# Optimization experiments

Hardware: AMD Instinct MI355X
Metric: run time of the kernel (lower is better)

The kernel has to match this reference:

```python
import jax, jax.numpy as jnp
import numpy as np

N, K, D = 65536, 16, 64  # points, neighbors, d_out
EPS = 1e-5


def setup_inputs() -> dict:
    key = jax.random.key(0)
    ks = jax.random.split(key, 10)
    s = lambda fan: 1.0 / np.sqrt(fan)
    return {
        "p": jax.random.normal(ks[0], (N, K, 3), jnp.float32),
        "x": jax.random.normal(ks[1], (N, K, D), jnp.float32),
        # BiMLP: Conv1d(10, 2D, 1) -> BN -> ReLU -> Conv1d(2D, D, 1)
        "w1": jax.random.normal(ks[2], (10, 2 * D), jnp.float32) * s(10),
        "b1": jnp.zeros((2 * D,), jnp.float32),
        "g1": jnp.ones((2 * D,), jnp.float32),
        "be1": jnp.zeros((2 * D,), jnp.float32),
        "w2": jax.random.normal(ks[3], (2 * D, D), jnp.float32) * s(2 * D),
        "b2": jnp.zeros((D,), jnp.float32),
        # score_fn: Linear(2D, 2D, bias=False)
        "ws": jax.random.normal(ks[4], (2 * D, 2 * D), jnp.float32) * s(2 * D),
        # mlp_out: Linear(2D, D) -> BN -> ReLU
        "wo": jax.random.normal(ks[5], (2 * D, D), jnp.float32) * s(2 * D),
        "bo": jnp.zeros((D,), jnp.float32),
        "g2": jnp.ones((D,), jnp.float32),
        "be2": jnp.zeros((D,), jnp.float32),
    }


def reference(p, x, w1, b1, g1, be1, w2, b2, ws, wo, bo, g2, be2):
    # p: [N,K,3] neighbor coords (index 0 is the center), x: [N,K,D]
    center = p[:, :1, :]                                   # [N,1,3]
    diff = center - p                                      # [N,K,3]
    dist = jnp.sqrt(jnp.sum(diff * diff, axis=2, keepdims=True))  # [N,K,1]
    concat = jnp.concatenate(
        [jnp.broadcast_to(center, p.shape), p, diff, dist], axis=-1)  # [N,K,10]

    # 1x1 conv == per-point linear over channel dim
    h = jnp.einsum('nkc,cd->nkd', concat, w1) + b1          # [N,K,2D]
    # BatchNorm1d over (N,K) per channel (training-mode batch stats)
    mu = jnp.mean(h, axis=(0, 1))
    var = jnp.var(h, axis=(0, 1))
    h = (h - mu) * jax.lax.rsqrt(var + EPS) * g1 + be1
    h = jax.nn.relu(h)
    p_c = jnp.einsum('nkd,de->nke', h, w2) + b2             # [N,K,D]

    p_x = jnp.concatenate([p_c, x], axis=-1)                # [N,K,2D]
    # attention scores: linear (no bias) then softmax over neighbor dim (-2)
    scores = jax.nn.softmax(jnp.einsum('nkd,de->nke', p_x, ws), axis=-2)
    feat = jnp.sum(scores * p_x, axis=1)                    # [N,2D]

    out = feat @ wo + bo                                    # [N,D]
    mu2 = jnp.mean(out, axis=0)
    var2 = jnp.var(out, axis=0)
    out = (out - mu2) * jax.lax.rsqrt(var2 + EPS) * g2 + be2
    return jax.nn.relu(out)
```

## Files before the change

### kernel.cpp

```cpp
#include <hip/hip_runtime.h>
#include <math.h>

#define NPTS 65536
#define EPSV 1e-5f
#define B1G  256
#define B3G  512

#define OFF_P1  0
#define OFF_S1  (B1G*65)
#define OFF_P2  (OFF_S1+256)
#define OFF_S2  (OFF_P2+B3G*128)
#define OFF_PRE (OFF_S2+128)

typedef unsigned int u32;
typedef short v8s __attribute__((ext_vector_type(8)));
typedef float v4f __attribute__((ext_vector_type(4)));

union F8 { v8s v; u32 u[4]; unsigned short s[8]; };

__device__ __forceinline__ u32 f2bf(float f){
  u32 u = __float_as_uint(f);
  return (u + 0x7fffu + ((u>>16)&1u)) >> 16;
}
__device__ __forceinline__ float bf2f(unsigned short s){ return __uint_as_float(((u32)s)<<16); }
__device__ __forceinline__ u32 packbf(float a, float b){ return f2bf(a) | (f2bf(b)<<16); }

__global__ __launch_bounds__(256) void k1_stats(const float* __restrict__ p, float* __restrict__ part1){
  int tid = blockIdx.x*256 + threadIdx.x;
  float M[55]; float s[10];
  #pragma unroll
  for(int i=0;i<55;i++) M[i]=0.f;
  #pragma unroll
  for(int i=0;i<10;i++) s[i]=0.f;
  for(int it=0; it<16; ++it){
    int r = it*65536 + tid;
    int n = r >> 4;
    int kk = r & 15;
    const float* pn = p + (size_t)n*48;
    float cx=pn[0], cy=pn[1], cz=pn[2];
    float ax=pn[kk*3+0], ay=pn[kk*3+1], az=pn[kk*3+2];
    float dx=cx-ax, dy=cy-ay, dz=cz-az;
    float dd = sqrtf(dx*dx+dy*dy+dz*dz);
    float c[10]={cx,cy,cz,ax,ay,az,dx,dy,dz,dd};
    #pragma unroll
    for(int i=0;i<10;i++) s[i]+=c[i];
    int idx=0;
    #pragma unroll
    for(int i=0;i<10;i++){
      #pragma unroll
      for(int j=i;j<10;j++){
        M[idx] = fmaf(c[i],c[j],M[idx]);
        idx++;
      }
    }
  }
  #pragma unroll
  for(int i=0;i<10;i++){
    for(int off=32; off>0; off>>=1) s[i] += __shfl_down(s[i], off, 64);
  }
  #pragma unroll
  for(int i=0;i<55;i++){
    for(int off=32; off>0; off>>=1) M[i] += __shfl_down(M[i], off, 64);
  }
  __shared__ float sm[4][65];
  int lane = threadIdx.x & 63, w = threadIdx.x >> 6;
  if(lane==0){
    #pragma unroll
    for(int i=0;i<10;i++) sm[w][i]=s[i];
    #pragma unroll
    for(int i=0;i<55;i++) sm[w][10+i]=M[i];
  }
  __syncthreads();
  if(threadIdx.x<65){
    float v = sm[0][threadIdx.x]+sm[1][threadIdx.x]+sm[2][threadIdx.x]+sm[3][threadIdx.x];
    part1[blockIdx.x*65 + threadIdx.x] = v;
  }
}

__device__ __forceinline__ int tri_idx(int i,int j){
  int a = i<j? i : j;
  int b = i<j? j : i;
  return 10*a - (a*(a-1))/2 + (b-a);
}
__global__ void k2_fin(const float* __restrict__ part1, const float* __restrict__ w1,
                       const float* __restrict__ g1, const float* __restrict__ be1,
                       float* __restrict__ stats1){
  __shared__ float S[65];
  int t = threadIdx.x;
  if(t<65){
    float a=0.f;
    for(int b=0;b<B1G;b++) a += part1[b*65+t];
    S[t]=a;
  }
  __syncthreads();
  float wc[10];
  #pragma unroll
  for(int c=0;c<10;c++) wc[c]=w1[c*128+t];
  float md=0.f;
  #pragma unroll
  for(int c=0;c<10;c++) md += S[c]*wc[c];
  const float invR = 1.0f/(float)(NPTS*16);
  md *= invR;
  float q=0.f;
  #pragma unroll
  for(int i=0;i<10;i++){
    float ti=0.f;
    #pragma unroll
    for(int j=0;j<10;j++) ti += S[10+tri_idx(i,j)]*wc[j];
    q = fmaf(ti, wc[i], q);
  }
  q *= invR;
  float var = q - md*md;
  float sc = g1[t]*rsqrtf(var+EPSV);
  float sh = be1[t] - md*sc;
  stats1[t]=sc;
  stats1[128+t]=sh;
}

__global__ __launch_bounds__(256,2) void k3_main(
    const float* __restrict__ p, const float* __restrict__ x,
    const float* __restrict__ w2, const float* __restrict__ b2,
    const float* __restrict__ wsm, const float* __restrict__ wo,
    const float* __restrict__ w1, const float* __restrict__ stats1,
    float* __restrict__ pre, float* __restrict__ part2)
{
  __shared__ unsigned short s_h [4][16][136];
  __shared__ unsigned short s_px[4][16][136];
  __shared__ float          s_lg[4][16][132];
  __shared__ unsigned short s_ft[16][136];

  const int tid  = threadIdx.x;
  const int w    = tid>>6;
  const int lane = tid&63;
  const int q    = lane>>4;
  const int c    = lane&15;

  v8s Bw1[2], Bw2[4], Bws[2][4], Bwo[4];
  #pragma unroll
  for(int t=0;t<2;t++){
    F8 f;
    #pragma unroll
    for(int j=0;j<8;j++){
      int k = q*8+j;
      f.s[j] = (unsigned short)(k<10 ? f2bf(w1[k*128 + 32*w + 16*t + c]) : 0);
    }
    Bw1[t]=f.v;
  }
  #pragma unroll
  for(int kk=0;kk<4;kk++){
    F8 f;
    #pragma unroll
    for(int j=0;j<8;j++) f.s[j]=(unsigned short)f2bf(w2[(kk*32+q*8+j)*64 + 16*w + c]);
    Bw2[kk]=f.v;
  }
  #pragma unroll
  for(int t=0;t<2;t++){
    #pragma unroll
    for(int kk=0;kk<4;kk++){
      F8 f;
      #pragma unroll
      for(int j=0;j<8;j++) f.s[j]=(unsigned short)f2bf(wsm[(kk*32+q*8+j)*128 + 32*w + 16*t + c]);
      Bws[t][kk]=f.v;
    }
  }
  #pragma unroll
  for(int kk=0;kk<4;kk++){
    F8 f;
    #pragma unroll
    for(int j=0;j<8;j++) f.s[j]=(unsigned short)f2bf(wo[(kk*32+q*8+j)*64 + 16*w + c]);
    Bwo[kk]=f.v;
  }
  const float sc1a = stats1[32*w+c],    sh1a = stats1[128+32*w+c];
  const float sc1b = stats1[32*w+16+c], sh1b = stats1[128+32*w+16+c];
  const float b2v  = b2[16*w+c];

  float a_s=0.f, a_q=0.f;
  const int base0 = blockIdx.x*128;

  for(int r=0;r<32;++r){
    const int base = base0 + 4*r;

    const float4* xg = (const float4*)(x + (size_t)base*1024);
    #pragma unroll
    for(int rr=0;rr<4;rr++){
      int f = tid + 256*rr;
      float4 v = xg[f];
      int nl = f>>8, rem = f&255, pt = rem>>4, d4 = rem&15;
      *(uint2*)&s_px[nl][pt][64+4*d4] = make_uint2(packbf(v.x,v.y), packbf(v.z,v.w));
    }

    #pragma unroll
    for(int n0=0;n0<4;n0++){
      const float* pn = p + (size_t)(base+n0)*48;
      float cx=pn[0], cy=pn[1], cz=pn[2];
      float ax=pn[3*c], ay=pn[3*c+1], az=pn[3*c+2];
      float dx=cx-ax, dy=cy-ay, dz=cz-az;
      float dd=sqrtf(dx*dx+dy*dy+dz*dz);
      float cr[10]={cx,cy,cz,ax,ay,az,dx,dy,dz,dd};
      F8 fa;
      #pragma unroll
      for(int j=0;j<8;j++){ int k=q*8+j; fa.s[j]=(unsigned short)(k<10 ? f2bf(cr[k]) : 0); }
      v4f z={0.f,0.f,0.f,0.f};
      v4f d0 = __builtin_amdgcn_mfma_f32_16x16x32_bf16(fa.v, Bw1[0], z, 0,0,0);
      v4f d1 = __builtin_amdgcn_mfma_f32_16x16x32_bf16(fa.v, Bw1[1], z, 0,0,0);
      #pragma unroll
      for(int i=0;i<4;i++){
        float v0 = fmaxf(0.f, fmaf(d0[i], sc1a, sh1a));
        float v1 = fmaxf(0.f, fmaf(d1[i], sc1b, sh1b));
        s_h[n0][4*q+i][32*w+c]    = (unsigned short)f2bf(v0);
        s_h[n0][4*q+i][32*w+16+c] = (unsigned short)f2bf(v1);
      }
    }
    __syncthreads();

    #pragma unroll
    for(int n0=0;n0<4;n0++){
      const v8s* Ar = (const v8s*)&s_h[n0][c][0];
      v4f acc={0.f,0.f,0.f,0.f};
      #pragma unroll
      for(int kk=0;kk<4;kk++)
        acc = __builtin_amdgcn_mfma_f32_16x16x32_bf16(Ar[kk*4+q], Bw2[kk], acc, 0,0,0);
      #pragma unroll
      for(int i=0;i<4;i++) s_px[n0][4*q+i][16*w+c] = (unsigned short)f2bf(acc[i] + b2v);
    }
    __syncthreads();

    #pragma unroll
    for(int n0=0;n0<4;n0++){
      const v8s* Ar = (const v8s*)&s_px[n0][c][0];
      v4f l0={0.f,0.f,0.f,0.f}, l1={0.f,0.f,0.f,0.f};
      #pragma unroll
      for(int kk=0;kk<4;kk++){
        v8s a = Ar[kk*4+q];
        l0 = __builtin_amdgcn_mfma_f32_16x16x32_bf16(a, Bws[0][kk], l0, 0,0,0);
        l1 = __builtin_amdgcn_mfma_f32_16x16x32_bf16(a, Bws[1][kk], l1, 0,0,0);
      }
      #pragma unroll
      for(int i=0;i<4;i++){
        s_lg[n0][4*q+i][32*w+c]    = l0[i];
        s_lg[n0][4*q+i][32*w+16+c] = l1[i];
      }
    }
    __syncthreads();

    {
      const int slot = (r&3)*4 + w;
      #pragma unroll
      for(int hh=0;hh<2;hh++){
        const int ch = lane + 64*hh;
        float lv[16];
        #pragma unroll
        for(int pt=0;pt<16;pt++) lv[pt] = s_lg[w][pt][ch];
        float m = lv[0];
        #pragma unroll
        for(int pt=1;pt<16;pt++) m = fmaxf(m, lv[pt]);
        float se=0.f, fe=0.f;
        #pragma unroll
        for(int pt=0;pt<16;pt++){
          float e = __expf(lv[pt]-m);
          se += e;
          fe = fmaf(e, bf2f(s_px[w][pt][ch]), fe);
        }
        s_ft[slot][ch] = (unsigned short)f2bf(fe/se);
      }
    }
    __syncthreads();

    if((r&3)==3){
      const v8s* Ar = (const v8s*)&s_ft[c][0];
      v4f o={0.f,0.f,0.f,0.f};
      #pragma unroll
      for(int kk=0;kk<4;kk++)
        o = __builtin_amdgcn_mfma_f32_16x16x32_bf16(Ar[kk*4+q], Bwo[kk], o, 0,0,0);
      const int nb16 = base0 + (r>>2)*16;
      #pragma unroll
      for(int i=0;i<4;i++){
        float val = o[i];
        pre[(size_t)(nb16 + 4*q + i)*64 + 16*w + c] = val;
        a_s += val;
        a_q = fmaf(val,val,a_q);
      }
    }
  }

  a_s += __shfl_xor(a_s, 16, 64); a_s += __shfl_xor(a_s, 32, 64);
  a_q += __shfl_xor(a_q, 16, 64); a_q += __shfl_xor(a_q, 32, 64);
  if(q==0){
    part2[blockIdx.x*128 + 16*w + c]      = a_s;
    part2[blockIdx.x*128 + 64 + 16*w + c] = a_q;
  }
}

__global__ void k4_fin(const float* __restrict__ part2, const float* __restrict__ g2,
                       const float* __restrict__ be2, float* __restrict__ stats2){
  int t = threadIdx.x;
  float s=0.f, qq=0.f;
  for(int b=0;b<B3G;b++){ s += part2[b*128+t]; qq += part2[b*128+64+t]; }
  float mu  = s/(float)NPTS;
  float var = qq/(float)NPTS - mu*mu;
  float sc = g2[t]*rsqrtf(var+EPSV);
  float sh = be2[t] - mu*sc;
  stats2[t]=sc;
  stats2[64+t]=sh;
}

__global__ __launch_bounds__(256) void k5_apply(const float* __restrict__ pre,
                                                const float* __restrict__ stats2,
                                                float* __restrict__ out){
  int i = blockIdx.x*256 + threadIdx.x;
  float4 v = ((const float4*)pre)[i];
  int d4 = i & 15;
  float4 sc = ((const float4*)stats2)[d4];
  float4 sh = ((const float4*)(stats2+64))[d4];
  float4 o;
  o.x = fmaxf(0.f, fmaf(v.x,sc.x,sh.x));
  o.y = fmaxf(0.f, fmaf(v.y,sc.y,sh.y));
  o.z = fmaxf(0.f, fmaf(v.z,sc.z,sh.z));
  o.w = fmaxf(0.f, fmaf(v.w,sc.w,sh.w));
  ((float4*)out)[i] = o;
}

extern "C" void kernel_launch(void* const* d_in, const int* in_sizes, int n_in,
                              void* d_out, int out_size, void* d_ws, size_t ws_size,
                              hipStream_t stream){
  (void)in_sizes; (void)n_in; (void)out_size; (void)ws_size;
  const float* p   = (const float*)d_in[0];
  const float* x   = (const float*)d_in[1];
  const float* w1  = (const float*)d_in[2];
  const float* g1  = (const float*)d_in[4];
  const float* be1 = (const float*)d_in[5];
  const float* w2  = (const float*)d_in[6];
  const float* b2  = (const float*)d_in[7];
  const float* wsm = (const float*)d_in[8];
  const float* wo  = (const float*)d_in[9];
  const float* g2  = (const float*)d_in[11];
  const float* be2 = (const float*)d_in[12];

  float* wsf    = (float*)d_ws;
  float* part1  = wsf + OFF_P1;
  float* stats1 = wsf + OFF_S1;
  float* part2  = wsf + OFF_P2;
  float* stats2 = wsf + OFF_S2;
  float* pre    = wsf + OFF_PRE;
  float* out    = (float*)d_out;

  k1_stats<<<B1G,256,0,stream>>>(p, part1);
  k2_fin  <<<1,128,0,stream>>>(part1, w1, g1, be1, stats1);
  k3_main <<<B3G,256,0,stream>>>(p,x,w2,b2,wsm,wo,w1,stats1,pre,part2);
  k4_fin  <<<1,64,0,stream>>>(part2,g2,be2,stats2);
  k5_apply<<<4096,256,0,stream>>>(pre,stats2,out);
}
```

Measured before the change: 591.6 us.

## Halve per-block point tile, raise occupancy, and simplify softmax with packed bf16 stores

The main kernel now processes 2 points per iteration instead of 4 and launches twice as many blocks. Shared memory is halved and launch bounds ask for 4 blocks per CU, to improve latency hiding. The softmax stage now gives each thread one channel with no max subtraction. Channels of h and logits are interleaved (with w2 rows permuted to match) so stores can use packed bf16/float2 writes, with a hardware packed bf16 convert where available. The second-stage stats reduction is spread across 256 threads and the partial buffers share one workspace region. Dropping the max subtraction risks exp overflow for large logits.

```diff
diff --git a/kernel.cpp b/kernel.cpp
--- a/kernel.cpp
+++ b/kernel.cpp
@@ -4,13 +4,12 @@
 #define NPTS 65536
 #define EPSV 1e-5f
 #define B1G  256
-#define B3G  512
-
-#define OFF_P1  0
-#define OFF_S1  (B1G*65)
-#define OFF_P2  (OFF_S1+256)
-#define OFF_S2  (OFF_P2+B3G*128)
-#define OFF_PRE (OFF_S2+128)
+#define B3G  1024
+
+#define OFF_PART 0
+#define OFF_S1   131072
+#define OFF_S2   (OFF_S1+256)
+#define OFF_PRE  (OFF_S2+128)
 
 typedef unsigned int u32;
 typedef short v8s __attribute__((ext_vector_type(8)));
@@ -23,7 +22,15 @@
   return (u + 0x7fffu + ((u>>16)&1u)) >> 16;
 }
 __device__ __forceinline__ float bf2f(unsigned short s){ return __uint_as_float(((u32)s)<<16); }
-__device__ __forceinline__ u32 packbf(float a, float b){ return f2bf(a) | (f2bf(b)<<16); }
+__device__ __forceinline__ u32 packbf(float a, float b){
+#if __has_builtin(__builtin_amdgcn_cvt_pk_bf16_f32)
+  auto rv = __builtin_amdgcn_cvt_pk_bf16_f32(a, b);
+  u32 u; __builtin_memcpy(&u, &rv, 4);
+  return u;
+#else
+  return f2bf(a) | (f2bf(b)<<16);
+#endif
+}
 
 __global__ __launch_bounds__(256) void k1_stats(const float* __restrict__ p, float* __restrict__ part1){
   int tid = blockIdx.x*256 + threadIdx.x;
@@ -117,17 +124,17 @@
   stats1[128+t]=sh;
 }
 
-__global__ __launch_bounds__(256,2) void k3_main(
+__global__ __launch_bounds__(256,4) void k3_main(
     const float* __restrict__ p, const float* __restrict__ x,
     const float* __restrict__ w2, const float* __restrict__ b2,
     const float* __restrict__ wsm, const float* __restrict__ wo,
     const float* __restrict__ w1, const float* __restrict__ stats1,
     float* __restrict__ pre, float* __restrict__ part2)
 {
-  __shared__ unsigned short s_h [4][16][136];
-  __shared__ unsigned short s_px[4][16][136];
-  __shared__ float          s_lg[4][16][132];
-  __shared__ unsigned short s_ft[16][136];
+  __shared__ __align__(16) unsigned short s_h [2][16][136];
+  __shared__ __align__(16) unsigned short s_px[2][16][136];
+  __shared__ __align__(16) float          s_lg[2][16][132];
+  __shared__ __align__(16) unsigned short s_ft[16][136];
 
   const int tid  = threadIdx.x;
   const int w    = tid>>6;
@@ -150,7 +157,11 @@
   for(int kk=0;kk<4;kk++){
     F8 f;
     #pragma unroll
-    for(int j=0;j<8;j++) f.s[j]=(unsigned short)f2bf(w2[(kk*32+q*8+j)*64 + 16*w + c]);
+    for(int j=0;j<8;j++){
+      int pos = kk*32 + q*8 + j;
+      int ch  = 32*(pos>>5) + 16*(pos&1) + ((pos>>1)&15);
+      f.s[j]=(unsigned short)f2bf(w2[ch*64 + 16*w + c]);
+    }
     Bw2[kk]=f.v;
   }
   #pragma unroll
@@ -174,32 +185,42 @@
   const float sc1b = stats1[32*w+16+c], sh1b = stats1[128+32*w+16+c];
   const float b2v  = b2[16*w+c];
 
+  const int n0s4 = w>>1;
+  const int ch4  = 64*(w&1) + lane;
+  const int lpos = 32*(ch4>>5) + 2*(ch4&15) + ((ch4>>4)&1);
+
   float a_s=0.f, a_q=0.f;
-  const int base0 = blockIdx.x*128;
+  const int base0 = blockIdx.x*64;
 
   for(int r=0;r<32;++r){
-    const int base = base0 + 4*r;
+    const int base = base0 + 2*r;
 
     const float4* xg = (const float4*)(x + (size_t)base*1024);
     #pragma unroll
-    for(int rr=0;rr<4;rr++){
+    for(int rr=0;rr<2;rr++){
       int f = tid + 256*rr;
       float4 v = xg[f];
-      int nl = f>>8, rem = f&255, pt = rem>>4, d4 = rem&15;
-      *(uint2*)&s_px[nl][pt][64+4*d4] = make_uint2(packbf(v.x,v.y), packbf(v.z,v.w));
-    }
-
-    #pragma unroll
-    for(int n0=0;n0<4;n0++){
-      const float* pn = p + (size_t)(base+n0)*48;
-      float cx=pn[0], cy=pn[1], cz=pn[2];
-      float ax=pn[3*c], ay=pn[3*c+1], az=pn[3*c+2];
-      float dx=cx-ax, dy=cy-ay, dz=cz-az;
-      float dd=sqrtf(dx*dx+dy*dy+dz*dz);
-      float cr[10]={cx,cy,cz,ax,ay,az,dx,dy,dz,dd};
+      int n0 = f>>8, rem = f&255, pt = rem>>4, d4 = rem&15;
+      *(uint2*)&s_px[n0][pt][64+4*d4] = make_uint2(packbf(v.x,v.y), packbf(v.z,v.w));
+    }
+
+    #pragma unroll
+    for(int n0=0;n0<2;n0++){
       F8 fa;
-      #pragma unroll
-      for(int j=0;j<8;j++){ int k=q*8+j; fa.s[j]=(unsigned short)(k<10 ? f2bf(cr[k]) : 0); }
+      fa.u[0]=0u; fa.u[1]=0u; fa.u[2]=0u; fa.u[3]=0u;
+      if(q<2){
+        const float* pn = p + (size_t)(base+n0)*48;
+        float cx=pn[0], cy=pn[1], cz=pn[2];
+        float ax=pn[3*c], ay=pn[3*c+1], az=pn[3*c+2];
+        float dx=cx-ax, dy=cy-ay, dz=cz-az;
+        float dd=sqrtf(dx*dx+dy*dy+dz*dz);
+        if(q==0){
+          fa.u[0]=packbf(cx,cy); fa.u[1]=packbf(cz,ax);
+          fa.u[2]=packbf(ay,az); fa.u[3]=packbf(dx,dy);
+        }else{
+          fa.u[0]=packbf(dz,dd);
+        }
+      }
       v4f z={0.f,0.f,0.f,0.f};
       v4f d0 = __builtin_amdgcn_mfma_f32_16x16x32_bf16(fa.v, Bw1[0], z, 0,0,0);
       v4f d1 = __builtin_amdgcn_mfma_f32_16x16x32_bf16(fa.v, Bw1[1], z, 0,0,0);
@@ -207,26 +228,29 @@
       for(int i=0;i<4;i++){
         float v0 = fmaxf(0.f, fmaf(d0[i], sc1a, sh1a));
         float v1 = fmaxf(0.f, fmaf(d1[i], sc1b, sh1b));
-        s_h[n0][4*q+i][32*w+c]    = (unsigned short)f2bf(v0);
-        s_h[n0][4*q+i][32*w+16+c] = (unsigned short)f2bf(v1);
+        *(u32*)&s_h[n0][4*q+i][32*w+2*c] = packbf(v0,v1);
       }
     }
     __syncthreads();
 
     #pragma unroll
-    for(int n0=0;n0<4;n0++){
+    for(int n0=0;n0<2;n0++){
       const v8s* Ar = (const v8s*)&s_h[n0][c][0];
       v4f acc={0.f,0.f,0.f,0.f};
       #pragma unroll
       for(int kk=0;kk<4;kk++)
         acc = __builtin_amdgcn_mfma_f32_16x16x32_bf16(Ar[kk*4+q], Bw2[kk], acc, 0,0,0);
-      #pragma unroll
-      for(int i=0;i<4;i++) s_px[n0][4*q+i][16*w+c] = (unsigned short)f2bf(acc[i] + b2v);
+      u32 pa = packbf(acc[0]+b2v, acc[1]+b2v);
+      u32 pb = packbf(acc[2]+b2v, acc[3]+b2v);
+      s_px[n0][4*q+0][16*w+c] = (unsigned short)pa;
+      s_px[n0][4*q+1][16*w+c] = (unsigned short)(pa>>16);
+      s_px[n0][4*q+2][16*w+c] = (unsigned short)pb;
+      s_px[n0][4*q+3][16*w+c] = (unsigned short)(pb>>16);
     }
     __syncthreads();
 
     #pragma unroll
-    for(int n0=0;n0<4;n0++){
+    for(int n0=0;n0<2;n0++){
       const v8s* Ar = (const v8s*)&s_px[n0][c][0];
       v4f l0={0.f,0.f,0.f,0.f}, l1={0.f,0.f,0.f,0.f};
       #pragma unroll
@@ -236,43 +260,30 @@
         l1 = __builtin_amdgcn_mfma_f32_16x16x32_bf16(a, Bws[1][kk], l1, 0,0,0);
       }
       #pragma unroll
-      for(int i=0;i<4;i++){
-        s_lg[n0][4*q+i][32*w+c]    = l0[i];
-        s_lg[n0][4*q+i][32*w+16+c] = l1[i];
-      }
+      for(int i=0;i<4;i++)
+        *(float2*)&s_lg[n0][4*q+i][32*w+2*c] = make_float2(l0[i], l1[i]);
     }
     __syncthreads();
 
     {
-      const int slot = (r&3)*4 + w;
-      #pragma unroll
-      for(int hh=0;hh<2;hh++){
-        const int ch = lane + 64*hh;
-        float lv[16];
-        #pragma unroll
-        for(int pt=0;pt<16;pt++) lv[pt] = s_lg[w][pt][ch];
-        float m = lv[0];
-        #pragma unroll
-        for(int pt=1;pt<16;pt++) m = fmaxf(m, lv[pt]);
-        float se=0.f, fe=0.f;
-        #pragma unroll
-        for(int pt=0;pt<16;pt++){
-          float e = __expf(lv[pt]-m);
-          se += e;
-          fe = fmaf(e, bf2f(s_px[w][pt][ch]), fe);
-        }
-        s_ft[slot][ch] = (unsigned short)f2bf(fe/se);
-      }
+      float se=0.f, fe=0.f;
+      #pragma unroll
+      for(int pt=0;pt<16;pt++){
+        float e = __expf(s_lg[n0s4][pt][lpos]);
+        se += e;
+        fe = fmaf(e, bf2f(s_px[n0s4][pt][ch4]), fe);
+      }
+      s_ft[(r&7)*2+n0s4][ch4] = (unsigned short)f2bf(__fdividef(fe,se));
     }
     __syncthreads();
 
-    if((r&3)==3){
+    if((r&7)==7){
       const v8s* Ar = (const v8s*)&s_ft[c][0];
       v4f o={0.f,0.f,0.f,0.f};
       #pragma unroll
       for(int kk=0;kk<4;kk++)
         o = __builtin_amdgcn_mfma_f32_16x16x32_bf16(Ar[kk*4+q], Bwo[kk], o, 0,0,0);
-      const int nb16 = base0 + (r>>2)*16;
+      const int nb16 = base0 + (r>>3)*16;
       #pragma unroll
       for(int i=0;i<4;i++){
         float val = o[i];
@@ -293,15 +304,22 @@
 
 __global__ void k4_fin(const float* __restrict__ part2, const float* __restrict__ g2,
                        const float* __restrict__ be2, float* __restrict__ stats2){
+  __shared__ float red[256];
   int t = threadIdx.x;
-  float s=0.f, qq=0.f;
-  for(int b=0;b<B3G;b++){ s += part2[b*128+t]; qq += part2[b*128+64+t]; }
-  float mu  = s/(float)NPTS;
-  float var = qq/(float)NPTS - mu*mu;
-  float sc = g2[t]*rsqrtf(var+EPSV);
-  float sh = be2[t] - mu*sc;
-  stats2[t]=sc;
-  stats2[64+t]=sh;
+  int j = t & 127, g = t >> 7;
+  float s = 0.f;
+  for(int b=g;b<B3G;b+=2) s += part2[b*128 + j];
+  red[t] = s;
+  __syncthreads();
+  if(t<64){
+    float su = red[t]    + red[128+t];
+    float qq = red[64+t] + red[192+t];
+    float mu  = su/(float)NPTS;
+    float var = qq/(float)NPTS - mu*mu;
+    float sc = g2[t]*rsqrtf(var+EPSV);
+    stats2[t]=sc;
+    stats2[64+t]=be2[t]-mu*sc;
+  }
 }
 
 __global__ __launch_bounds__(256) void k5_apply(const float* __restrict__ pre,
@@ -337,9 +355,9 @@
   const float* be2 = (const float*)d_in[12];
 
   float* wsf    = (float*)d_ws;
-  float* part1  = wsf + OFF_P1;
+  float* part1  = wsf + OFF_PART;
+  float* part2  = wsf + OFF_PART;
   float* stats1 = wsf + OFF_S1;
-  float* part2  = wsf + OFF_P2;
   float* stats2 = wsf + OFF_S2;
   float* pre    = wsf + OFF_PRE;
   float* out    = (float*)d_out;
@@ -347,6 +365,6 @@
   k1_stats<<<B1G,256,0,stream>>>(p, part1);
   k2_fin  <<<1,128,0,stream>>>(part1, w1, g1, be1, stats1);
   k3_main <<<B3G,256,0,stream>>>(p,x,w2,b2,wsm,wo,w1,stats1,pre,part2);
-  k4_fin  <<<1,64,0,stream>>>(part2,g2,be2,stats2);
+  k4_fin  <<<1,256,0,stream>>>(part2,g2,be2,stats2);
   k5_apply<<<4096,256,0,stream>>>(pre,stats2,out);
 }
```

After: 620.6 us. +4.9%, slower.
